# Performance work log

Measured on AMD Instinct MI355X. Metric: run time of the kernel, lower is better.

Reference implementation:

```python
import jax, jax.numpy as jnp
import numpy as np

IC, OC, ID, OD = 1152, 10, 8, 16   # input_caps, output_caps, input_dim, output_dim
N_ITER = 5
THRESHOLD = 1e-05
EPS = 1e-20


def setup_inputs() -> dict:
    key = jax.random.key(0)
    k1, k2 = jax.random.split(key)
    x = jax.random.uniform(k1, (32, IC, ID), dtype=jnp.float32)
    # replicate CapsLayer.__init__ + norm_weights(): uniform(0,1), normalize over
    # output_caps dim, clamp to threshold, renormalize
    w = jax.random.uniform(k2, (IC, OC, ID, OD), dtype=jnp.float32)
    w = w / (w.sum(axis=1, keepdims=True) + EPS)
    w = jnp.clip(w, THRESHOLD, None)
    w = w / (w.sum(axis=1, keepdims=True) + EPS)
    return {"x": x, "weights": w}


def nnmf_sbs(inp, weights):
    # inp: [B, ic, id], weights: [ic, oc, id, od] -> out: [B, ic, oc, od]
    B = inp.shape[0]
    out0 = jnp.full((B, IC, OC, OD), 1.0 / OD, dtype=inp.dtype)

    def body(out, _):
        h_w = out[:, :, :, None, :] * weights[None]          # [B,ic,oc,id,od]
        h_w = h_w / (h_w.sum(-1, keepdims=True) + EPS)       # normalize over od
        h_w = (h_w * inp[:, :, None, :, None]).sum(-2)       # reduce id -> [B,ic,oc,od]
        out = h_w / (h_w.sum(-1, keepdims=True) + EPS)       # normalize over od
        return out, None

    out, _ = jax.lax.scan(body, out0, None, length=N_ITER)
    return out


def reference(x, weights):
    x = x / (x.sum(-1, keepdims=True) + EPS)                 # normalize over input_dim
    h = nnmf_sbs(x, weights)                                 # [B,ic,oc,od]
    # reconstruct = (h.unsqueeze(-2) * weights).sum(-1) -> [B,ic,oc,id]
    reconstruct = jnp.einsum('bicd,iced->bice', h, weights)
    alpha = jnp.einsum('bice,bie->bic', reconstruct, x)      # [B,ic,oc]
    alpha = alpha / (alpha.sum(-1, keepdims=True) + EPS)     # normalize over oc
    return jnp.einsum('bicd,bic->bcd', h, alpha)             # sum over ic -> [B,oc,od]
```

## Files before the change

### kernel.cpp

```cpp
#include <hip/hip_runtime.h>

#define B_   32
#define ICN  1152
#define OCN  10
#define IDN  8
#define ODN  16
#define ODH  8
#define NIT  5
#define EPS  1e-20f
#define OUTN (B_ * OCN * ODN)
#define BGRP 11
#define NBLK (BGRP * ICN)

typedef float v4f __attribute__((ext_vector_type(4)));

__device__ __forceinline__ float dpp_swap1(float x) {
  return __int_as_float(__builtin_amdgcn_update_dpp(
      0, __float_as_int(x), 0xB1, 0xF, 0xF, true));
}

__device__ __forceinline__ v4f gload4(const float* p) {
  v4f r;
  asm volatile("global_load_dwordx4 %0, %1, off" : "=v"(r) : "v"(p));
  return r;
}

__global__ __launch_bounds__(64, 2) void caps_main(
    const float* __restrict__ xg, const float* __restrict__ wg,
    float* __restrict__ ws) {
  const int l = threadIdx.x;
  const int bid = blockIdx.x;
  const int ic = bid % ICN;
  const int bgrp = bid / ICN;
  const int grp = l / 20;
  const int q = l % 20;
  const int oc = q >> 1;
  const int half = q & 1;
  const int b = bgrp * 3 + grp;
  const bool valid = (grp < 3) && (b < B_);
  const int bb = (b < B_) ? b : (B_ - 1);

  v4f wv[2 * IDN];
  {
    const float* wp = wg + ((size_t)ic * OCN + oc) * (IDN * ODN) + half * ODH;
#pragma unroll
    for (int id = 0; id < IDN; ++id) {
      wv[2 * id]     = gload4(wp + id * ODN);
      wv[2 * id + 1] = gload4(wp + id * ODN + 4);
    }
  }
  v4f xv0, xv1;
  {
    const float* xp = xg + ((size_t)bb * ICN + ic) * IDN;
    xv0 = gload4(xp);
    xv1 = gload4(xp + 4);
  }
  asm volatile("s_waitcnt vmcnt(0)" ::: "memory");
  __builtin_amdgcn_sched_barrier(0);

#define W(id, k) (wv[2 * (id) + ((k) >> 2)][(k) & 3])

  float xn[IDN];
  {
    xn[0] = xv0.x; xn[1] = xv0.y; xn[2] = xv0.z; xn[3] = xv0.w;
    xn[4] = xv1.x; xn[5] = xv1.y; xn[6] = xv1.z; xn[7] = xv1.w;
    const float s = ((xn[0] + xn[1]) + (xn[2] + xn[3])) +
                    ((xn[4] + xn[5]) + (xn[6] + xn[7]));
    const float r = __builtin_amdgcn_rcpf(s + EPS);
#pragma unroll
    for (int i = 0; i < IDN; ++i) xn[i] *= r;
  }

  float h[ODH];
#pragma unroll
  for (int k = 0; k < ODH; ++k) h[k] = 1.0f / ODN;

#pragma unroll 1
  for (int it = 0; it < NIT; ++it) {
    float pd[IDN];
#pragma unroll
    for (int id = 0; id < IDN; ++id) {
      float p = 0.f;
#pragma unroll
      for (int k = 0; k < ODH; ++k) p = fmaf(h[k], W(id, k), p);
      pd[id] = p;
    }
    float tc[IDN];
#pragma unroll
    for (int id = 0; id < IDN; ++id) {
      const float den = pd[id] + dpp_swap1(pd[id]);
      tc[id] = xn[id] * __builtin_amdgcn_rcpf(den + EPS);
    }
    float hacc[ODH];
#pragma unroll
    for (int k = 0; k < ODH; ++k) hacc[k] = W(0, k) * tc[0];
#pragma unroll
    for (int id = 1; id < IDN; ++id)
#pragma unroll
      for (int k = 0; k < ODH; ++k) hacc[k] = fmaf(W(id, k), tc[id], hacc[k]);
#pragma unroll
    for (int k = 0; k < ODH; ++k) h[k] *= hacc[k];
    const float ps = ((h[0] + h[1]) + (h[2] + h[3])) +
                     ((h[4] + h[5]) + (h[6] + h[7]));
    const float hs = ps + dpp_swap1(ps);
    const float r = __builtin_amdgcn_rcpf(hs + EPS);
#pragma unroll
    for (int k = 0; k < ODH; ++k) h[k] *= r;
  }

  float ap = 0.f;
#pragma unroll
  for (int id = 0; id < IDN; ++id) {
    float rec = 0.f;
#pragma unroll
    for (int k = 0; k < ODH; ++k) rec = fmaf(h[k], W(id, k), rec);
    ap = fmaf(rec, xn[id], ap);
  }
  const float af = ap + dpp_swap1(ap);
  float asum = 0.f;
  const int gbase = grp * 20;
#pragma unroll
  for (int k = 0; k < OCN; ++k) asum += __shfl(af, gbase + 2 * k, 64);
  const float an = af * __builtin_amdgcn_rcpf(asum + EPS);

  if (valid) {
    float* dst = ws + (size_t)ic * OUTN + (bb * OCN + oc) * ODN + half * ODH;
    float4 v0, v1;
    v0.x = h[0] * an; v0.y = h[1] * an; v0.z = h[2] * an; v0.w = h[3] * an;
    v1.x = h[4] * an; v1.y = h[5] * an; v1.z = h[6] * an; v1.w = h[7] * an;
    ((float4*)dst)[0] = v0;
    ((float4*)dst)[1] = v1;
  }
#undef W
}

__global__ __launch_bounds__(64, 2) void caps_main_atomic(
    const float* __restrict__ xg, const float* __restrict__ wg,
    float* __restrict__ outg) {
  const int l = threadIdx.x;
  const int bid = blockIdx.x;
  const int ic = bid % ICN;
  const int bgrp = bid / ICN;
  const int grp = l / 20;
  const int q = l % 20;
  const int oc = q >> 1;
  const int half = q & 1;
  const int b = bgrp * 3 + grp;
  const bool valid = (grp < 3) && (b < B_);
  const int bb = (b < B_) ? b : (B_ - 1);

  float wr[IDN][ODH];
  {
    const float* wp = wg + ((size_t)ic * OCN + oc) * (IDN * ODN) + half * ODH;
#pragma unroll
    for (int id = 0; id < IDN; ++id) {
      const float4 v0 = *(const float4*)(wp + id * ODN);
      const float4 v1 = *(const float4*)(wp + id * ODN + 4);
      wr[id][0] = v0.x; wr[id][1] = v0.y; wr[id][2] = v0.z; wr[id][3] = v0.w;
      wr[id][4] = v1.x; wr[id][5] = v1.y; wr[id][6] = v1.z; wr[id][7] = v1.w;
    }
  }
  float xn[IDN];
  {
    const float* xp = xg + ((size_t)bb * ICN + ic) * IDN;
    const float4 a0 = ((const float4*)xp)[0];
    const float4 a1 = ((const float4*)xp)[1];
    xn[0] = a0.x; xn[1] = a0.y; xn[2] = a0.z; xn[3] = a0.w;
    xn[4] = a1.x; xn[5] = a1.y; xn[6] = a1.z; xn[7] = a1.w;
    float s = 0.f;
#pragma unroll
    for (int i = 0; i < IDN; ++i) s += xn[i];
    const float r = __builtin_amdgcn_rcpf(s + EPS);
#pragma unroll
    for (int i = 0; i < IDN; ++i) xn[i] *= r;
  }
  float h[ODH];
#pragma unroll
  for (int k = 0; k < ODH; ++k) h[k] = 1.0f / ODN;
#pragma unroll 1
  for (int it = 0; it < NIT; ++it) {
    float pd[IDN];
#pragma unroll
    for (int id = 0; id < IDN; ++id) {
      float p = 0.f;
#pragma unroll
      for (int k = 0; k < ODH; ++k) p = fmaf(h[k], wr[id][k], p);
      pd[id] = p;
    }
    float tc[IDN];
#pragma unroll
    for (int id = 0; id < IDN; ++id) {
      const float den = pd[id] + dpp_swap1(pd[id]);
      tc[id] = xn[id] * __builtin_amdgcn_rcpf(den + EPS);
    }
    float hacc[ODH];
#pragma unroll
    for (int k = 0; k < ODH; ++k) hacc[k] = wr[0][k] * tc[0];
#pragma unroll
    for (int id = 1; id < IDN; ++id)
#pragma unroll
      for (int k = 0; k < ODH; ++k) hacc[k] = fmaf(wr[id][k], tc[id], hacc[k]);
#pragma unroll
    for (int k = 0; k < ODH; ++k) h[k] *= hacc[k];
    float ps = 0.f;
#pragma unroll
    for (int k = 0; k < ODH; ++k) ps += h[k];
    const float hs = ps + dpp_swap1(ps);
    const float r = __builtin_amdgcn_rcpf(hs + EPS);
#pragma unroll
    for (int k = 0; k < ODH; ++k) h[k] *= r;
  }
  float ap = 0.f;
#pragma unroll
  for (int id = 0; id < IDN; ++id) {
    float rec = 0.f;
#pragma unroll
    for (int k = 0; k < ODH; ++k) rec = fmaf(h[k], wr[id][k], rec);
    ap = fmaf(rec, xn[id], ap);
  }
  const float af = ap + dpp_swap1(ap);
  float asum = 0.f;
  const int gbase = grp * 20;
#pragma unroll
  for (int k = 0; k < OCN; ++k) asum += __shfl(af, gbase + 2 * k, 64);
  const float an = af * __builtin_amdgcn_rcpf(asum + EPS);
  if (valid) {
    const int base = (bb * OCN + oc) * ODN + half * ODH;
#pragma unroll
    for (int k = 0; k < ODH; ++k) atomicAdd(outg + base + k, h[k] * an);
  }
}

#define RSPLIT 32
#define RROWS  (ICN / RSPLIT)
__global__ void caps_reduce(const float* __restrict__ ws, float* __restrict__ outg) {
  const int j = blockIdx.x * 256 + threadIdx.x;
  const int r0 = blockIdx.y * RROWS;
  float s = 0.f;
#pragma unroll
  for (int r = 0; r < RROWS; ++r) s += ws[(size_t)(r0 + r) * OUTN + j];
  atomicAdd(outg + j, s);
}

extern "C" void kernel_launch(void* const* d_in, const int* in_sizes, int n_in,
                              void* d_out, int out_size, void* d_ws, size_t ws_size,
                              hipStream_t stream) {
  const float* x = (const float*)d_in[0];
  const float* w = (const float*)d_in[1];
  float* out = (float*)d_out;
  float* ws = (float*)d_ws;

  hipMemsetAsync(out, 0, OUTN * sizeof(float), stream);

  const size_t need = (size_t)ICN * OUTN * sizeof(float);

  if (ws_size >= need) {
    caps_main<<<NBLK, 64, 0, stream>>>(x, w, ws);
    caps_reduce<<<dim3(OUTN / 256, RSPLIT), 256, 0, stream>>>(ws, out);
  } else {
    caps_main_atomic<<<NBLK, 64, 0, stream>>>(x, w, out);
  }
}
```

Baseline: 91.20 us.

## Process two input capsules per block and accumulate partials in registers

Each block now loops over two input capsules and sums their weighted contributions in registers before writing one partial row. This halves the workspace written by the main kernel and the rows read by the reduce kernel, and halves the block count. It also drops the inline-asm vector loads and explicit waitcnt in favour of plain float4 loads and raises the launch-bounds occupancy hint from 2 to 4. The cost is that each block runs its two capsules serially, with fewer blocks available to hide latency.

```diff
diff --git a/kernel.cpp b/kernel.cpp
--- a/kernel.cpp
+++ b/kernel.cpp
@@ -10,28 +10,22 @@
 #define EPS  1e-20f
 #define OUTN (B_ * OCN * ODN)
 #define BGRP 11
-#define NBLK (BGRP * ICN)
-
-typedef float v4f __attribute__((ext_vector_type(4)));
+#define GIC  2
+#define NGRP (ICN / GIC)
+#define NBLK (BGRP * NGRP)
 
 __device__ __forceinline__ float dpp_swap1(float x) {
   return __int_as_float(__builtin_amdgcn_update_dpp(
       0, __float_as_int(x), 0xB1, 0xF, 0xF, true));
 }
 
-__device__ __forceinline__ v4f gload4(const float* p) {
-  v4f r;
-  asm volatile("global_load_dwordx4 %0, %1, off" : "=v"(r) : "v"(p));
-  return r;
-}
-
-__global__ __launch_bounds__(64, 2) void caps_main(
+__global__ __launch_bounds__(64, 4) void caps_main(
     const float* __restrict__ xg, const float* __restrict__ wg,
     float* __restrict__ ws) {
   const int l = threadIdx.x;
   const int bid = blockIdx.x;
-  const int ic = bid % ICN;
-  const int bgrp = bid / ICN;
+  const int wgrp = bid % NGRP;
+  const int bgrp = bid / NGRP;
   const int grp = l / 20;
   const int q = l % 20;
   const int oc = q >> 1;
@@ -39,108 +33,115 @@
   const int b = bgrp * 3 + grp;
   const bool valid = (grp < 3) && (b < B_);
   const int bb = (b < B_) ? b : (B_ - 1);
-
-  v4f wv[2 * IDN];
-  {
-    const float* wp = wg + ((size_t)ic * OCN + oc) * (IDN * ODN) + half * ODH;
+  const int ic0 = wgrp * GIC;
+
+  float oacc[ODH];
+#pragma unroll
+  for (int k = 0; k < ODH; ++k) oacc[k] = 0.f;
+
+#pragma unroll 1
+  for (int g = 0; g < GIC; ++g) {
+    const int ic = ic0 + g;
+
+    float wr[IDN][ODH];
+    {
+      const float* wp = wg + ((size_t)ic * OCN + oc) * (IDN * ODN) + half * ODH;
+#pragma unroll
+      for (int id = 0; id < IDN; ++id) {
+        const float4 v0 = *(const float4*)(wp + id * ODN);
+        const float4 v1 = *(const float4*)(wp + id * ODN + 4);
+        wr[id][0] = v0.x; wr[id][1] = v0.y; wr[id][2] = v0.z; wr[id][3] = v0.w;
+        wr[id][4] = v1.x; wr[id][5] = v1.y; wr[id][6] = v1.z; wr[id][7] = v1.w;
+      }
+    }
+
+    float xn[IDN];
+    {
+      const float* xp = xg + ((size_t)bb * ICN + ic) * IDN;
+      const float4 a0 = ((const float4*)xp)[0];
+      const float4 a1 = ((const float4*)xp)[1];
+      xn[0] = a0.x; xn[1] = a0.y; xn[2] = a0.z; xn[3] = a0.w;
+      xn[4] = a1.x; xn[5] = a1.y; xn[6] = a1.z; xn[7] = a1.w;
+      const float s = ((xn[0] + xn[1]) + (xn[2] + xn[3])) +
+                      ((xn[4] + xn[5]) + (xn[6] + xn[7]));
+      const float r = __builtin_amdgcn_rcpf(s + EPS);
+#pragma unroll
+      for (int i = 0; i < IDN; ++i) xn[i] *= r;
+    }
+
+    float h[ODH];
+#pragma unroll
+    for (int k = 0; k < ODH; ++k) h[k] = 1.0f / ODN;
+
+#pragma unroll 1
+    for (int it = 0; it < NIT; ++it) {
+      float pd[IDN];
+#pragma unroll
+      for (int id = 0; id < IDN; ++id) {
+        float p = 0.f;
+#pragma unroll
+        for (int k = 0; k < ODH; ++k) p = fmaf(h[k], wr[id][k], p);
+        pd[id] = p;
+      }
+      float tc[IDN];
+#pragma unroll
+      for (int id = 0; id < IDN; ++id) {
+        const float den = pd[id] + dpp_swap1(pd[id]);
+        tc[id] = xn[id] * __builtin_amdgcn_rcpf(den + EPS);
+      }
+      float hacc[ODH];
+#pragma unroll
+      for (int k = 0; k < ODH; ++k) hacc[k] = wr[0][k] * tc[0];
+#pragma unroll
+      for (int id = 1; id < IDN; ++id)
+#pragma unroll
+        for (int k = 0; k < ODH; ++k) hacc[k] = fmaf(wr[id][k], tc[id], hacc[k]);
+#pragma unroll
+      for (int k = 0; k < ODH; ++k) h[k] *= hacc[k];
+      const float ps = ((h[0] + h[1]) + (h[2] + h[3])) +
+                       ((h[4] + h[5]) + (h[6] + h[7]));
+      const float hs = ps + dpp_swap1(ps);
+      const float r = __builtin_amdgcn_rcpf(hs + EPS);
+#pragma unroll
+      for (int k = 0; k < ODH; ++k) h[k] *= r;
+    }
+
+    float ap = 0.f;
 #pragma unroll
     for (int id = 0; id < IDN; ++id) {
-      wv[2 * id]     = gload4(wp + id * ODN);
-      wv[2 * id + 1] = gload4(wp + id * ODN + 4);
-    }
-  }
-  v4f xv0, xv1;
-  {
-    const float* xp = xg + ((size_t)bb * ICN + ic) * IDN;
-    xv0 = gload4(xp);
-    xv1 = gload4(xp + 4);
-  }
-  asm volatile("s_waitcnt vmcnt(0)" ::: "memory");
-  __builtin_amdgcn_sched_barrier(0);
-
-#define W(id, k) (wv[2 * (id) + ((k) >> 2)][(k) & 3])
-
-  float xn[IDN];
-  {
-    xn[0] = xv0.x; xn[1] = xv0.y; xn[2] = xv0.z; xn[3] = xv0.w;
-    xn[4] = xv1.x; xn[5] = xv1.y; xn[6] = xv1.z; xn[7] = xv1.w;
-    const float s = ((xn[0] + xn[1]) + (xn[2] + xn[3])) +
-                    ((xn[4] + xn[5]) + (xn[6] + xn[7]));
-    const float r = __builtin_amdgcn_rcpf(s + EPS);
-#pragma unroll
-    for (int i = 0; i < IDN; ++i) xn[i] *= r;
-  }
-
-  float h[ODH];
-#pragma unroll
-  for (int k = 0; k < ODH; ++k) h[k] = 1.0f / ODN;
-
-#pragma unroll 1
-  for (int it = 0; it < NIT; ++it) {
-    float pd[IDN];
-#pragma unroll
-    for (int id = 0; id < IDN; ++id) {
-      float p = 0.f;
-#pragma unroll
-      for (int k = 0; k < ODH; ++k) p = fmaf(h[k], W(id, k), p);
-      pd[id] = p;
-    }
-    float tc[IDN];
-#pragma unroll
-    for (int id = 0; id < IDN; ++id) {
-      const float den = pd[id] + dpp_swap1(pd[id]);
-      tc[id] = xn[id] * __builtin_amdgcn_rcpf(den + EPS);
-    }
-    float hacc[ODH];
-#pragma unroll
-    for (int k = 0; k < ODH; ++k) hacc[k] = W(0, k) * tc[0];
-#pragma unroll
-    for (int id = 1; id < IDN; ++id)
-#pragma unroll
-      for (int k = 0; k < ODH; ++k) hacc[k] = fmaf(W(id, k), tc[id], hacc[k]);
-#pragma unroll
-    for (int k = 0; k < ODH; ++k) h[k] *= hacc[k];
-    const float ps = ((h[0] + h[1]) + (h[2] + h[3])) +
-                     ((h[4] + h[5]) + (h[6] + h[7]));
-    const float hs = ps + dpp_swap1(ps);
-    const float r = __builtin_amdgcn_rcpf(hs + EPS);
-#pragma unroll
-    for (int k = 0; k < ODH; ++k) h[k] *= r;
-  }
-
-  float ap = 0.f;
-#pragma unroll
-  for (int id = 0; id < IDN; ++id) {
-    float rec = 0.f;
-#pragma unroll
-    for (int k = 0; k < ODH; ++k) rec = fmaf(h[k], W(id, k), rec);
-    ap = fmaf(rec, xn[id], ap);
-  }
-  const float af = ap + dpp_swap1(ap);
-  float asum = 0.f;
-  const int gbase = grp * 20;
-#pragma unroll
-  for (int k = 0; k < OCN; ++k) asum += __shfl(af, gbase + 2 * k, 64);
-  const float an = af * __builtin_amdgcn_rcpf(asum + EPS);
+      float rec = 0.f;
+#pragma unroll
+      for (int k = 0; k < ODH; ++k) rec = fmaf(h[k], wr[id][k], rec);
+      ap = fmaf(rec, xn[id], ap);
+    }
+    const float af = ap + dpp_swap1(ap);
+    float asum = 0.f;
+    const int gbase = grp * 20;
+#pragma unroll
+    for (int k = 0; k < OCN; ++k) asum += __shfl(af, gbase + 2 * k, 64);
+    const float an = af * __builtin_amdgcn_rcpf(asum + EPS);
+
+#pragma unroll
+    for (int k = 0; k < ODH; ++k) oacc[k] = fmaf(h[k], an, oacc[k]);
+  }
 
   if (valid) {
-    float* dst = ws + (size_t)ic * OUTN + (bb * OCN + oc) * ODN + half * ODH;
+    float* dst = ws + (size_t)wgrp * OUTN + (bb * OCN + oc) * ODN + half * ODH;
     float4 v0, v1;
-    v0.x = h[0] * an; v0.y = h[1] * an; v0.z = h[2] * an; v0.w = h[3] * an;
-    v1.x = h[4] * an; v1.y = h[5] * an; v1.z = h[6] * an; v1.w = h[7] * an;
+    v0.x = oacc[0]; v0.y = oacc[1]; v0.z = oacc[2]; v0.w = oacc[3];
+    v1.x = oacc[4]; v1.y = oacc[5]; v1.z = oacc[6]; v1.w = oacc[7];
     ((float4*)dst)[0] = v0;
     ((float4*)dst)[1] = v1;
   }
-#undef W
-}
-
-__global__ __launch_bounds__(64, 2) void caps_main_atomic(
+}
+
+__global__ __launch_bounds__(64, 4) void caps_main_atomic(
     const float* __restrict__ xg, const float* __restrict__ wg,
     float* __restrict__ outg) {
   const int l = threadIdx.x;
   const int bid = blockIdx.x;
-  const int ic = bid % ICN;
-  const int bgrp = bid / ICN;
+  const int wgrp = bid % NGRP;
+  const int bgrp = bid / NGRP;
   const int grp = l / 20;
   const int q = l % 20;
   const int oc = q >> 1;
@@ -148,91 +149,102 @@
   const int b = bgrp * 3 + grp;
   const bool valid = (grp < 3) && (b < B_);
   const int bb = (b < B_) ? b : (B_ - 1);
-
-  float wr[IDN][ODH];
-  {
-    const float* wp = wg + ((size_t)ic * OCN + oc) * (IDN * ODN) + half * ODH;
+  const int ic0 = wgrp * GIC;
+
+  float oacc[ODH];
+#pragma unroll
+  for (int k = 0; k < ODH; ++k) oacc[k] = 0.f;
+
+#pragma unroll 1
+  for (int g = 0; g < GIC; ++g) {
+    const int ic = ic0 + g;
+    float wr[IDN][ODH];
+    {
+      const float* wp = wg + ((size_t)ic * OCN + oc) * (IDN * ODN) + half * ODH;
+#pragma unroll
+      for (int id = 0; id < IDN; ++id) {
+        const float4 v0 = *(const float4*)(wp + id * ODN);
+        const float4 v1 = *(const float4*)(wp + id * ODN + 4);
+        wr[id][0] = v0.x; wr[id][1] = v0.y; wr[id][2] = v0.z; wr[id][3] = v0.w;
+        wr[id][4] = v1.x; wr[id][5] = v1.y; wr[id][6] = v1.z; wr[id][7] = v1.w;
+      }
+    }
+    float xn[IDN];
+    {
+      const float* xp = xg + ((size_t)bb * ICN + ic) * IDN;
+      const float4 a0 = ((const float4*)xp)[0];
+      const float4 a1 = ((const float4*)xp)[1];
+      xn[0] = a0.x; xn[1] = a0.y; xn[2] = a0.z; xn[3] = a0.w;
+      xn[4] = a1.x; xn[5] = a1.y; xn[6] = a1.z; xn[7] = a1.w;
+      float s = 0.f;
+#pragma unroll
+      for (int i = 0; i < IDN; ++i) s += xn[i];
+      const float r = __builtin_amdgcn_rcpf(s + EPS);
+#pragma unroll
+      for (int i = 0; i < IDN; ++i) xn[i] *= r;
+    }
+    float h[ODH];
+#pragma unroll
+    for (int k = 0; k < ODH; ++k) h[k] = 1.0f / ODN;
+#pragma unroll 1
+    for (int it = 0; it < NIT; ++it) {
+      float pd[IDN];
+#pragma unroll
+      for (int id = 0; id < IDN; ++id) {
+        float p = 0.f;
+#pragma unroll
+        for (int k = 0; k < ODH; ++k) p = fmaf(h[k], wr[id][k], p);
+        pd[id] = p;
+      }
+      float tc[IDN];
+#pragma unroll
+      for (int id = 0; id < IDN; ++id) {
+        const float den = pd[id] + dpp_swap1(pd[id]);
+        tc[id] = xn[id] * __builtin_amdgcn_rcpf(den + EPS);
+      }
+      float hacc[ODH];
+#pragma unroll
+      for (int k = 0; k < ODH; ++k) hacc[k] = wr[0][k] * tc[0];
+#pragma unroll
+      for (int id = 1; id < IDN; ++id)
+#pragma unroll
+        for (int k = 0; k < ODH; ++k) hacc[k] = fmaf(wr[id][k], tc[id], hacc[k]);
+#pragma unroll
+      for (int k = 0; k < ODH; ++k) h[k] *= hacc[k];
+      float ps = 0.f;
+#pragma unroll
+      for (int k = 0; k < ODH; ++k) ps += h[k];
+      const float hs = ps + dpp_swap1(ps);
+      const float r = __builtin_amdgcn_rcpf(hs + EPS);
+#pragma unroll
+      for (int k = 0; k < ODH; ++k) h[k] *= r;
+    }
+    float ap = 0.f;
 #pragma unroll
     for (int id = 0; id < IDN; ++id) {
-      const float4 v0 = *(const float4*)(wp + id * ODN);
-      const float4 v1 = *(const float4*)(wp + id * ODN + 4);
-      wr[id][0] = v0.x; wr[id][1] = v0.y; wr[id][2] = v0.z; wr[id][3] = v0.w;
-      wr[id][4] = v1.x; wr[id][5] = v1.y; wr[id][6] = v1.z; wr[id][7] = v1.w;
-    }
-  }
-  float xn[IDN];
-  {
-    const float* xp = xg + ((size_t)bb * ICN + ic) * IDN;
-    const float4 a0 = ((const float4*)xp)[0];
-    const float4 a1 = ((const float4*)xp)[1];
-    xn[0] = a0.x; xn[1] = a0.y; xn[2] = a0.z; xn[3] = a0.w;
-    xn[4] = a1.x; xn[5] = a1.y; xn[6] = a1.z; xn[7] = a1.w;
-    float s = 0.f;
-#pragma unroll
-    for (int i = 0; i < IDN; ++i) s += xn[i];
-    const float r = __builtin_amdgcn_rcpf(s + EPS);
-#pragma unroll
-    for (int i = 0; i < IDN; ++i) xn[i] *= r;
-  }
-  float h[ODH];
-#pragma unroll
-  for (int k = 0; k < ODH; ++k) h[k] = 1.0f / ODN;
-#pragma unroll 1
-  for (int it = 0; it < NIT; ++it) {
-    float pd[IDN];
-#pragma unroll
-    for (int id = 0; id < IDN; ++id) {
-      float p = 0.f;
-#pragma unroll
-      for (int k = 0; k < ODH; ++k) p = fmaf(h[k], wr[id][k], p);
-      pd[id] = p;
-    }
-    float tc[IDN];
-#pragma unroll
-    for (int id = 0; id < IDN; ++id) {
-      const float den = pd[id] + dpp_swap1(pd[id]);
-      tc[id] = xn[id] * __builtin_amdgcn_rcpf(den + EPS);
-    }
-    float hacc[ODH];
-#pragma unroll
-    for (int k = 0; k < ODH; ++k) hacc[k] = wr[0][k] * tc[0];
-#pragma unroll
-    for (int id = 1; id < IDN; ++id)
-#pragma unroll
-      for (int k = 0; k < ODH; ++k) hacc[k] = fmaf(wr[id][k], tc[id], hacc[k]);
-#pragma unroll
-    for (int k = 0; k < ODH; ++k) h[k] *= hacc[k];
-    float ps = 0.f;
-#pragma unroll
-    for (int k = 0; k < ODH; ++k) ps += h[k];
-    const float hs = ps + dpp_swap1(ps);
-    const float r = __builtin_amdgcn_rcpf(hs + EPS);
-#pragma unroll
-    for (int k = 0; k < ODH; ++k) h[k] *= r;
-  }
-  float ap = 0.f;
-#pragma unroll
-  for (int id = 0; id < IDN; ++id) {
-    float rec = 0.f;
-#pragma unroll
-    for (int k = 0; k < ODH; ++k) rec = fmaf(h[k], wr[id][k], rec);
-    ap = fmaf(rec, xn[id], ap);
-  }
-  const float af = ap + dpp_swap1(ap);
-  float asum = 0.f;
-  const int gbase = grp * 20;
-#pragma unroll
-  for (int k = 0; k < OCN; ++k) asum += __shfl(af, gbase + 2 * k, 64);
-  const float an = af * __builtin_amdgcn_rcpf(asum + EPS);
+      float rec = 0.f;
+#pragma unroll
+      for (int k = 0; k < ODH; ++k) rec = fmaf(h[k], wr[id][k], rec);
+      ap = fmaf(rec, xn[id], ap);
+    }
+    const float af = ap + dpp_swap1(ap);
+    float asum = 0.f;
+    const int gbase = grp * 20;
+#pragma unroll
+    for (int k = 0; k < OCN; ++k) asum += __shfl(af, gbase + 2 * k, 64);
+    const float an = af * __builtin_amdgcn_rcpf(asum + EPS);
+#pragma unroll
+    for (int k = 0; k < ODH; ++k) oacc[k] = fmaf(h[k], an, oacc[k]);
+  }
   if (valid) {
     const int base = (bb * OCN + oc) * ODN + half * ODH;
 #pragma unroll
-    for (int k = 0; k < ODH; ++k) atomicAdd(outg + base + k, h[k] * an);
-  }
-}
-
-#define RSPLIT 32
-#define RROWS  (ICN / RSPLIT)
+    for (int k = 0; k < ODH; ++k) atomicAdd(outg + base + k, oacc[k]);
+  }
+}
+
+#define RSPLIT 16
+#define RROWS  (NGRP / RSPLIT)
 __global__ void caps_reduce(const float* __restrict__ ws, float* __restrict__ outg) {
   const int j = blockIdx.x * 256 + threadIdx.x;
   const int r0 = blockIdx.y * RROWS;
@@ -252,7 +264,7 @@
 
   hipMemsetAsync(out, 0, OUTN * sizeof(float), stream);
 
-  const size_t need = (size_t)ICN * OUTN * sizeof(float);
+  const size_t need = (size_t)NGRP * OUTN * sizeof(float);
 
   if (ws_size >= need) {
     caps_main<<<NBLK, 64, 0, stream>>>(x, w, ws);
```

After: 89.80 us. Within noise of the previous version (-1.5%).
